# Kernel tuning notes

Hardware: AMD Instinct MI355X
Metric: run time of the kernel (lower is better)

Reference implementation:

```python
import jax, jax.numpy as jnp
import numpy as np

N = 50000      # nodes
E = 800000     # edges per relation
D_IN = 128
D_OUT = 128


def setup_inputs() -> dict:
    key = jax.random.key(0)
    ks = jax.random.split(key, 9)
    feat = jax.random.normal(ks[0], (N, D_IN), dtype=jnp.float32)
    src0 = jax.random.randint(ks[1], (E,), 0, N)
    dst0 = jax.random.randint(ks[2], (E,), 0, N)
    src1 = jax.random.randint(ks[3], (E,), 0, N)
    dst1 = jax.random.randint(ks[4], (E,), 0, N)
    s = 1.0 / np.sqrt(D_IN)
    W0 = jax.random.uniform(ks[5], (D_IN, D_OUT), jnp.float32, -s, s)
    b0 = jax.random.uniform(ks[6], (D_OUT,), jnp.float32, -s, s)
    W1 = jax.random.uniform(ks[7], (D_IN, D_OUT), jnp.float32, -s, s)
    b1 = jax.random.uniform(ks[8], (D_OUT,), jnp.float32, -s, s)
    return {"feat": feat, "W0": W0, "b0": b0, "W1": W1, "b1": b1,
            "src0": src0, "dst0": dst0, "src1": src1, "dst1": dst1}


def _rel_mean(Wh, src, dst):
    # copy_u('Wh','m') + mean('m','h'): gather src features, mean over in-edges per dst
    msg = Wh[src]                                  # [E, D_OUT] irregular gather
    summ = jax.ops.segment_sum(msg, dst, num_segments=N)
    cnt = jax.ops.segment_sum(jnp.ones((msg.shape[0],), Wh.dtype), dst, num_segments=N)
    return summ / jnp.maximum(cnt, 1.0)[:, None]   # isolated dst nodes -> 0


def reference(feat, W0, b0, W1, b1, src0, dst0, src1, dst1):
    Wh0 = feat @ W0 + b0                           # per-etype linear on src features
    Wh1 = feat @ W1 + b1
    h = _rel_mean(Wh0, src0, dst0) + _rel_mean(Wh1, src1, dst1)  # 'sum' cross-reducer
    return h
```

## Files before the change

### kernel.cpp

```cpp
#include <hip/hip_runtime.h>
#include <hip/hip_fp16.h>

#define N_NODES 50000
#define N_EDGES 800000
#define DIM 128
#define NPB 64
#define NB 782
#define BCAP 1344
#define CHUNK 4096
#define GROWS 64

__global__ __launch_bounds__(512) void bin_kernel(
    const int* __restrict__ src0, const int* __restrict__ dst0,
    const int* __restrict__ src1, const int* __restrict__ dst1,
    int* __restrict__ gcur, unsigned* __restrict__ staging) {
    __shared__ int hist[NB], base[NB], curs[NB], gbase[NB];
    __shared__ int wtot[8], wbase[8];
    __shared__ unsigned stageRec[CHUNK];
    __shared__ int tgt[CHUNK];

    int t = threadIdx.x;
    const int nchunks = (N_EDGES + CHUNK - 1) / CHUNK;
    int rel = blockIdx.x >= nchunks;
    int ci  = rel ? blockIdx.x - nchunks : blockIdx.x;
    const int* src = rel ? src1 : src0;
    const int* dst = rel ? dst1 : dst0;
    int e0 = ci * CHUNK;
    int n = N_EDGES - e0; if (n > CHUNK) n = CHUNK;

    for (int i = t; i < NB; i += 512) hist[i] = 0;
    __syncthreads();

    for (int i = t; i < n; i += 512) {
        int d = dst[e0 + i];
        atomicAdd(&hist[d >> 6], 1);
    }
    __syncthreads();

    {
        int i0 = t * 2;
        int s0 = (i0 < NB) ? hist[i0] : 0;
        int s1 = (i0 + 1 < NB) ? hist[i0 + 1] : 0;
        int v = s0 + s1;
        int lane = t & 63, w = t >> 6;
        int x = v;
        #pragma unroll
        for (int dd = 1; dd < 64; dd <<= 1) {
            int u = __shfl_up(x, dd);
            if (lane >= dd) x += u;
        }
        if (lane == 63) wtot[w] = x;
        __syncthreads();
        if (t == 0) {
            int s = 0;
            #pragma unroll
            for (int j = 0; j < 8; ++j) { wbase[j] = s; s += wtot[j]; }
        }
        __syncthreads();
        int excl = wbase[w] + x - v;
        if (i0 < NB)     { base[i0] = excl;          curs[i0] = excl; }
        if (i0 + 1 < NB) { base[i0 + 1] = excl + s0; curs[i0 + 1] = excl + s0; }
    }
    __syncthreads();
    for (int i = t; i < NB; i += 512) {
        int c = hist[i];
        gbase[i] = c ? atomicAdd(&gcur[rel * NB + i], c) : 0;
    }
    __syncthreads();

    for (int i = t; i < n; i += 512) {
        int s = src[e0 + i];
        int d = dst[e0 + i];
        int bkt = d >> 6;
        int pos = atomicAdd(&curs[bkt], 1);
        int j = pos - base[bkt];
        int go = gbase[bkt] + j;
        stageRec[pos] = ((unsigned)s << 6) | (unsigned)(d & 63);
        tgt[pos] = (go < BCAP) ? (rel * NB + bkt) * BCAP + go : -1;
    }
    __syncthreads();

    for (int i = t; i < n; i += 512) {
        int a = tgt[i];
        if (a >= 0) staging[a] = stageRec[i];
    }
}

__global__ __launch_bounds__(256) void gemm_kernel(const float* __restrict__ feat,
                                                   const float* __restrict__ W0,
                                                   const float* __restrict__ b0,
                                                   const float* __restrict__ W1,
                                                   const float* __restrict__ b1,
                                                   __half* __restrict__ Wh0,
                                                   __half* __restrict__ Wh1) {
    __shared__ float fs[GROWS][DIM];
    int tx = threadIdx.x;
    int ty = threadIdx.y;
    int t = ty * 32 + tx;
    int row0 = blockIdx.x * GROWS;
    int nrows = N_NODES - row0; if (nrows > GROWS) nrows = GROWS;

    const float4* fsrc = (const float4*)(feat + (size_t)row0 * DIM);
    float4* fdst = (float4*)(&fs[0][0]);
    int nf4 = nrows * (DIM / 4);
    #pragma unroll
    for (int j = 0; j < 8; ++j) {
        int idx = t + j * 256;
        if (idx < nf4) fdst[idx] = fsrc[idx];
    }
    __syncthreads();

    int c4 = tx * 4;
    float4 acc0[8], acc1[8];
    #pragma unroll
    for (int r = 0; r < 8; ++r) {
        acc0[r] = make_float4(0.f, 0.f, 0.f, 0.f);
        acc1[r] = make_float4(0.f, 0.f, 0.f, 0.f);
    }

    #pragma unroll 2
    for (int k = 0; k < DIM; ++k) {
        float4 w0 = *(const float4*)(W0 + k * DIM + c4);
        float4 w1 = *(const float4*)(W1 + k * DIM + c4);
        #pragma unroll
        for (int r = 0; r < 8; ++r) {
            float f = fs[ty * 8 + r][k];
            acc0[r].x += f * w0.x; acc0[r].y += f * w0.y;
            acc0[r].z += f * w0.z; acc0[r].w += f * w0.w;
            acc1[r].x += f * w1.x; acc1[r].y += f * w1.y;
            acc1[r].z += f * w1.z; acc1[r].w += f * w1.w;
        }
    }

    float4 bb0 = *(const float4*)(b0 + c4);
    float4 bb1 = *(const float4*)(b1 + c4);
    #pragma unroll
    for (int r = 0; r < 8; ++r) {
        int row = row0 + ty * 8 + r;
        if (row < N_NODES) {
            __half2 p0 = __floats2half2_rn(acc0[r].x + bb0.x, acc0[r].y + bb0.y);
            __half2 p1 = __floats2half2_rn(acc0[r].z + bb0.z, acc0[r].w + bb0.w);
            uint2 pk;
            pk.x = *(unsigned*)&p0; pk.y = *(unsigned*)&p1;
            *(uint2*)(Wh0 + (size_t)row * DIM + c4) = pk;
            p0 = __floats2half2_rn(acc1[r].x + bb1.x, acc1[r].y + bb1.y);
            p1 = __floats2half2_rn(acc1[r].z + bb1.z, acc1[r].w + bb1.w);
            pk.x = *(unsigned*)&p0; pk.y = *(unsigned*)&p1;
            *(uint2*)(Wh1 + (size_t)row * DIM + c4) = pk;
        }
    }
}

__device__ inline float4 cvt8(uint2 r) {
    __half2 h0, h1;
    *(unsigned*)&h0 = r.x; *(unsigned*)&h1 = r.y;
    float2 f0 = __half22float2(h0), f1 = __half22float2(h1);
    return make_float4(f0.x, f0.y, f1.x, f1.y);
}

__global__ __launch_bounds__(512) void pull2_kernel(
    const unsigned* __restrict__ staging, const int* __restrict__ gcur,
    const __half* __restrict__ Wh0, const __half* __restrict__ Wh1,
    float* __restrict__ out) {
    __shared__ int srt[2][BCAP];
    __shared__ int hist2[2][NPB], off2[2][NPB], cur2[2][NPB];

    int b = blockIdx.x;
    int t = threadIdx.x;
    int nb0 = b * NPB;
    int n_nodes = N_NODES - nb0; if (n_nodes > NPB) n_nodes = NPB;

    int c0 = gcur[b];       if (c0 > BCAP) c0 = BCAP;
    int c1 = gcur[NB + b];  if (c1 > BCAP) c1 = BCAP;
    const unsigned* st0 = staging + (size_t)b * BCAP;
    const unsigned* st1 = staging + (size_t)(NB + b) * BCAP;

    if (t < 2 * NPB) ((int*)hist2)[t] = 0;
    __syncthreads();

    for (int i = t; i < c0; i += 512) atomicAdd(&hist2[0][st0[i] & 63], 1);
    for (int i = t; i < c1; i += 512) atomicAdd(&hist2[1][st1[i] & 63], 1);
    __syncthreads();

    if (t < 2 * NPB) {
        int r = t >> 6, l = t & 63;
        int v = hist2[r][l];
        int x = v;
        #pragma unroll
        for (int dd = 1; dd < 64; dd <<= 1) {
            int u = __shfl_up(x, dd);
            if (l >= dd) x += u;
        }
        off2[r][l] = x - v;
        cur2[r][l] = x - v;
    }
    __syncthreads();

    for (int i = t; i < c0; i += 512) {
        unsigned rec = st0[i];
        int pos = atomicAdd(&cur2[0][rec & 63], 1);
        srt[0][pos] = (int)(rec >> 6);
    }
    for (int i = t; i < c1; i += 512) {
        unsigned rec = st1[i];
        int pos = atomicAdd(&cur2[1][rec & 63], 1);
        srt[1][pos] = (int)(rec >> 6);
    }
    __syncthreads();

    int wv = t >> 6, lane = t & 63;
    int hf = lane >> 5;
    int col = (lane & 31) * 4;
    for (int l = wv; l < n_nodes; l += 8) {
        float4 o4 = make_float4(0.f, 0.f, 0.f, 0.f);
        #pragma unroll
        for (int r = 0; r < 2; ++r) {
            const __half* Wh = r ? Wh1 : Wh0;
            int c = hist2[r][l], ob = off2[r][l];
            float4 a = make_float4(0.f, 0.f, 0.f, 0.f);
            float4 bb = make_float4(0.f, 0.f, 0.f, 0.f);
            int i = 0;
            for (; i + 8 <= c; i += 8) {
                int s0 = srt[r][ob + i + hf];
                int s1 = srt[r][ob + i + 2 + hf];
                int s2 = srt[r][ob + i + 4 + hf];
                int s3 = srt[r][ob + i + 6 + hf];
                float4 v0 = cvt8(*(const uint2*)(Wh + (size_t)s0 * DIM + col));
                float4 v1 = cvt8(*(const uint2*)(Wh + (size_t)s1 * DIM + col));
                float4 v2 = cvt8(*(const uint2*)(Wh + (size_t)s2 * DIM + col));
                float4 v3 = cvt8(*(const uint2*)(Wh + (size_t)s3 * DIM + col));
                a.x += v0.x; a.y += v0.y; a.z += v0.z; a.w += v0.w;
                bb.x += v1.x; bb.y += v1.y; bb.z += v1.z; bb.w += v1.w;
                a.x += v2.x; a.y += v2.y; a.z += v2.z; a.w += v2.w;
                bb.x += v3.x; bb.y += v3.y; bb.z += v3.z; bb.w += v3.w;
            }
            for (; i < c; i += 2) {
                int e = i + hf;
                if (e < c) {
                    int s = srt[r][ob + e];
                    float4 v = cvt8(*(const uint2*)(Wh + (size_t)s * DIM + col));
                    a.x += v.x; a.y += v.y; a.z += v.z; a.w += v.w;
                }
            }
            a.x += bb.x; a.y += bb.y; a.z += bb.z; a.w += bb.w;
            float f = 1.0f / (float)(c > 0 ? c : 1);
            o4.x += a.x * f; o4.y += a.y * f; o4.z += a.z * f; o4.w += a.w * f;
        }
        o4.x += __shfl_xor(o4.x, 32);
        o4.y += __shfl_xor(o4.y, 32);
        o4.z += __shfl_xor(o4.z, 32);
        o4.w += __shfl_xor(o4.w, 32);
        if (hf == 0) {
            *(float4*)(out + (size_t)(nb0 + l) * DIM + col) = o4;
        }
    }
}

extern "C" void kernel_launch(void* const* d_in, const int* in_sizes, int n_in,
                              void* d_out, int out_size, void* d_ws, size_t ws_size,
                              hipStream_t stream) {
    const float* feat = (const float*)d_in[0];
    const float* W0   = (const float*)d_in[1];
    const float* b0   = (const float*)d_in[2];
    const float* W1   = (const float*)d_in[3];
    const float* b1   = (const float*)d_in[4];
    const int* src0   = (const int*)d_in[5];
    const int* dst0   = (const int*)d_in[6];
    const int* src1   = (const int*)d_in[7];
    const int* dst1   = (const int*)d_in[8];
    float* out = (float*)d_out;

    char* ws = (char*)d_ws;
    size_t o = 0;
    auto carve = [&](size_t bytes) {
        void* p = ws + o;
        o += (bytes + 255) & ~size_t(255);
        return p;
    };
    __half* Wh0      = (__half*)carve(sizeof(__half) * N_NODES * DIM);
    __half* Wh1      = (__half*)carve(sizeof(__half) * N_NODES * DIM);
    unsigned* staging = (unsigned*)carve(sizeof(unsigned) * 2 * NB * BCAP);
    int* gcur        = (int*)carve(sizeof(int) * 2 * NB);

    hipMemsetAsync(gcur, 0, sizeof(int) * 2 * NB, stream);

    const int nchunks = (N_EDGES + CHUNK - 1) / CHUNK;
    bin_kernel<<<2 * nchunks, 512, 0, stream>>>(src0, dst0, src1, dst1,
                                                gcur, staging);
    gemm_kernel<<<(N_NODES + GROWS - 1) / GROWS, dim3(32, 8), 0, stream>>>(
        feat, W0, b0, W1, b1, Wh0, Wh1);
    pull2_kernel<<<NB, 512, 0, stream>>>(staging, gcur, Wh0, Wh1, out);
}
```

Baseline: 241.9 us.

## Use MFMA fp16 for the linear layer and split aggregation blocks in half

The scalar FP32 GEMM becomes an MFMA 16x16x32 f16 kernel. A new pack kernel converts W0/W1 into fragment-ordered half8 tiles, feature rows are converted to fp16 fragments in LDS, and outputs are staged through LDS for coalesced stores. The pull kernel now launches two 256-thread blocks per 64-node bucket, each handling 32 destination nodes and filtering records by half, which raises block count but reads each staging bucket twice. Input features are now rounded to fp16 before the multiply, which costs precision, and the smaller HCAP may drop edges if one half overflows.

Result: faster. 195.6 us (-19.1%).

```diff
diff --git a/kernel.cpp b/kernel.cpp
--- a/kernel.cpp
+++ b/kernel.cpp
@@ -7,8 +7,11 @@
 #define NPB 64
 #define NB 782
 #define BCAP 1344
+#define HCAP 768
 #define CHUNK 4096
-#define GROWS 64
+
+typedef _Float16 half8 __attribute__((ext_vector_type(8)));
+typedef float f32x4 __attribute__((ext_vector_type(4)));
 
 __global__ __launch_bounds__(512) void bin_kernel(
     const int* __restrict__ src0, const int* __restrict__ dst0,
@@ -86,67 +89,118 @@
     }
 }
 
+__global__ __launch_bounds__(256) void wpack_kernel(const float* __restrict__ W0,
+                                                    const float* __restrict__ W1,
+                                                    half8* __restrict__ Bp) {
+    int tid = blockIdx.x * 256 + threadIdx.x;
+    int lane = tid & 63;
+    int nt = (tid >> 6) & 7;
+    int ks = (tid >> 9) & 3;
+    int rel = (tid >> 11) & 1;
+    const float* W = rel ? W1 : W0;
+    int g = lane >> 4, r = lane & 15;
+    int n = nt * 16 + r;
+    half8 h;
+    #pragma unroll
+    for (int j = 0; j < 8; ++j) {
+        int k = ks * 32 + (j >> 2) * 16 + g * 4 + (j & 3);
+        h[j] = (_Float16)W[k * DIM + n];
+    }
+    Bp[tid] = h;
+}
+
 __global__ __launch_bounds__(256) void gemm_kernel(const float* __restrict__ feat,
-                                                   const float* __restrict__ W0,
+                                                   const half8* __restrict__ Bp,
                                                    const float* __restrict__ b0,
-                                                   const float* __restrict__ W1,
                                                    const float* __restrict__ b1,
                                                    __half* __restrict__ Wh0,
                                                    __half* __restrict__ Wh1) {
-    __shared__ float fs[GROWS][DIM];
-    int tx = threadIdx.x;
-    int ty = threadIdx.y;
-    int t = ty * 32 + tx;
-    int row0 = blockIdx.x * GROWS;
-    int nrows = N_NODES - row0; if (nrows > GROWS) nrows = GROWS;
+    __shared__ __align__(16) _Float16 Afrag[4 * 4 * 64 * 8];
+    __shared__ __align__(16) __half Otile[64 * DIM];
+
+    int t = threadIdx.x;
+    int row0 = blockIdx.x * 64;
+    int totalRows = N_NODES - row0; if (totalRows > 64) totalRows = 64;
 
     const float4* fsrc = (const float4*)(feat + (size_t)row0 * DIM);
-    float4* fdst = (float4*)(&fs[0][0]);
-    int nf4 = nrows * (DIM / 4);
-    #pragma unroll
-    for (int j = 0; j < 8; ++j) {
-        int idx = t + j * 256;
-        if (idx < nf4) fdst[idx] = fsrc[idx];
-    }
-    __syncthreads();
-
-    int c4 = tx * 4;
-    float4 acc0[8], acc1[8];
-    #pragma unroll
-    for (int r = 0; r < 8; ++r) {
-        acc0[r] = make_float4(0.f, 0.f, 0.f, 0.f);
-        acc1[r] = make_float4(0.f, 0.f, 0.f, 0.f);
-    }
-
-    #pragma unroll 2
-    for (int k = 0; k < DIM; ++k) {
-        float4 w0 = *(const float4*)(W0 + k * DIM + c4);
-        float4 w1 = *(const float4*)(W1 + k * DIM + c4);
-        #pragma unroll
-        for (int r = 0; r < 8; ++r) {
-            float f = fs[ty * 8 + r][k];
-            acc0[r].x += f * w0.x; acc0[r].y += f * w0.y;
-            acc0[r].z += f * w0.z; acc0[r].w += f * w0.w;
-            acc1[r].x += f * w1.x; acc1[r].y += f * w1.y;
-            acc1[r].z += f * w1.z; acc1[r].w += f * w1.w;
-        }
-    }
-
-    float4 bb0 = *(const float4*)(b0 + c4);
-    float4 bb1 = *(const float4*)(b1 + c4);
-    #pragma unroll
-    for (int r = 0; r < 8; ++r) {
-        int row = row0 + ty * 8 + r;
-        if (row < N_NODES) {
-            __half2 p0 = __floats2half2_rn(acc0[r].x + bb0.x, acc0[r].y + bb0.y);
-            __half2 p1 = __floats2half2_rn(acc0[r].z + bb0.z, acc0[r].w + bb0.w);
-            uint2 pk;
-            pk.x = *(unsigned*)&p0; pk.y = *(unsigned*)&p1;
-            *(uint2*)(Wh0 + (size_t)row * DIM + c4) = pk;
-            p0 = __floats2half2_rn(acc1[r].x + bb1.x, acc1[r].y + bb1.y);
-            p1 = __floats2half2_rn(acc1[r].z + bb1.z, acc1[r].w + bb1.w);
-            pk.x = *(unsigned*)&p0; pk.y = *(unsigned*)&p1;
-            *(uint2*)(Wh1 + (size_t)row * DIM + c4) = pk;
+    #pragma unroll
+    for (int i = 0; i < 8; ++i) {
+        int e = t + i * 256;
+        int row = e >> 5;
+        int kq = e & 31;
+        float4 v = (row < totalRows) ? fsrc[e] : make_float4(0.f, 0.f, 0.f, 0.f);
+        int ks = kq >> 3;
+        int g  = kq & 3;
+        int hi = (kq >> 2) & 1;
+        int wv = row >> 4, r = row & 15;
+        union { _Float16 h[4]; uint2 u; } p;
+        p.h[0] = (_Float16)v.x; p.h[1] = (_Float16)v.y;
+        p.h[2] = (_Float16)v.z; p.h[3] = (_Float16)v.w;
+        *(uint2*)((char*)Afrag + (((wv * 4 + ks) * 64 + g * 16 + r) * 16 + hi * 8)) = p.u;
+    }
+    __syncthreads();
+
+    int wv = t >> 6, l = t & 63;
+    half8 a[4];
+    #pragma unroll
+    for (int ks = 0; ks < 4; ++ks)
+        a[ks] = ((const half8*)Afrag)[(wv * 4 + ks) * 64 + l];
+
+    f32x4 acc0[8], acc1[8];
+    #pragma unroll
+    for (int nt = 0; nt < 8; ++nt) { acc0[nt] = (f32x4)0.f; acc1[nt] = (f32x4)0.f; }
+
+    #pragma unroll
+    for (int nt = 0; nt < 8; ++nt) {
+        #pragma unroll
+        for (int ks = 0; ks < 4; ++ks) {
+            half8 bf0 = Bp[(ks * 8 + nt) * 64 + l];
+            acc0[nt] = __builtin_amdgcn_mfma_f32_16x16x32_f16(a[ks], bf0, acc0[nt], 0, 0, 0);
+            half8 bf1 = Bp[((4 + ks) * 8 + nt) * 64 + l];
+            acc1[nt] = __builtin_amdgcn_mfma_f32_16x16x32_f16(a[ks], bf1, acc1[nt], 0, 0, 0);
+        }
+    }
+
+    int cR = l & 15, rG = l >> 4;
+    #pragma unroll
+    for (int nt = 0; nt < 8; ++nt) {
+        float bias = b0[nt * 16 + cR];
+        #pragma unroll
+        for (int reg = 0; reg < 4; ++reg) {
+            int rowL = rG * 4 + reg;
+            Otile[(wv * 16 + rowL) * DIM + nt * 16 + cR] = __float2half(acc0[nt][reg] + bias);
+        }
+    }
+    __syncthreads();
+    {
+        const uint4* ot = (const uint4*)Otile;
+        uint4* dst = (uint4*)(Wh0 + (size_t)row0 * DIM);
+        #pragma unroll
+        for (int i = 0; i < 4; ++i) {
+            int idx = t + i * 256;
+            int row = idx >> 4;
+            if (row < totalRows) dst[idx] = ot[idx];
+        }
+    }
+    __syncthreads();
+    #pragma unroll
+    for (int nt = 0; nt < 8; ++nt) {
+        float bias = b1[nt * 16 + cR];
+        #pragma unroll
+        for (int reg = 0; reg < 4; ++reg) {
+            int rowL = rG * 4 + reg;
+            Otile[(wv * 16 + rowL) * DIM + nt * 16 + cR] = __float2half(acc1[nt][reg] + bias);
+        }
+    }
+    __syncthreads();
+    {
+        const uint4* ot = (const uint4*)Otile;
+        uint4* dst = (uint4*)(Wh1 + (size_t)row0 * DIM);
+        #pragma unroll
+        for (int i = 0; i < 4; ++i) {
+            int idx = t + i * 256;
+            int row = idx >> 4;
+            if (row < totalRows) dst[idx] = ot[idx];
         }
     }
 }
@@ -158,36 +212,45 @@
     return make_float4(f0.x, f0.y, f1.x, f1.y);
 }
 
-__global__ __launch_bounds__(512) void pull2_kernel(
+__global__ __launch_bounds__(256) void pull2_kernel(
     const unsigned* __restrict__ staging, const int* __restrict__ gcur,
     const __half* __restrict__ Wh0, const __half* __restrict__ Wh1,
     float* __restrict__ out) {
-    __shared__ int srt[2][BCAP];
-    __shared__ int hist2[2][NPB], off2[2][NPB], cur2[2][NPB];
-
-    int b = blockIdx.x;
+    __shared__ int srt[2][HCAP];
+    __shared__ int hist2[2][32], off2[2][32], cur2[2][32];
+
+    int blk = blockIdx.x;
+    int b = blk >> 1, half = blk & 1;
     int t = threadIdx.x;
-    int nb0 = b * NPB;
-    int n_nodes = N_NODES - nb0; if (n_nodes > NPB) n_nodes = NPB;
+    int nb0 = b * NPB + half * 32;
+    int n_nodes = N_NODES - nb0;
+    if (n_nodes > 32) n_nodes = 32;
+    if (n_nodes < 0) n_nodes = 0;
 
     int c0 = gcur[b];       if (c0 > BCAP) c0 = BCAP;
     int c1 = gcur[NB + b];  if (c1 > BCAP) c1 = BCAP;
     const unsigned* st0 = staging + (size_t)b * BCAP;
     const unsigned* st1 = staging + (size_t)(NB + b) * BCAP;
 
-    if (t < 2 * NPB) ((int*)hist2)[t] = 0;
-    __syncthreads();
-
-    for (int i = t; i < c0; i += 512) atomicAdd(&hist2[0][st0[i] & 63], 1);
-    for (int i = t; i < c1; i += 512) atomicAdd(&hist2[1][st1[i] & 63], 1);
-    __syncthreads();
-
-    if (t < 2 * NPB) {
-        int r = t >> 6, l = t & 63;
+    if (t < 64) ((int*)hist2)[t] = 0;
+    __syncthreads();
+
+    for (int i = t; i < c0; i += 256) {
+        unsigned rec = st0[i]; int d = rec & 63;
+        if ((d >> 5) == half) atomicAdd(&hist2[0][d & 31], 1);
+    }
+    for (int i = t; i < c1; i += 256) {
+        unsigned rec = st1[i]; int d = rec & 63;
+        if ((d >> 5) == half) atomicAdd(&hist2[1][d & 31], 1);
+    }
+    __syncthreads();
+
+    if (t < 64) {
+        int r = t >> 5, l = t & 31;
         int v = hist2[r][l];
         int x = v;
         #pragma unroll
-        for (int dd = 1; dd < 64; dd <<= 1) {
+        for (int dd = 1; dd < 32; dd <<= 1) {
             int u = __shfl_up(x, dd);
             if (l >= dd) x += u;
         }
@@ -196,22 +259,26 @@
     }
     __syncthreads();
 
-    for (int i = t; i < c0; i += 512) {
-        unsigned rec = st0[i];
-        int pos = atomicAdd(&cur2[0][rec & 63], 1);
-        srt[0][pos] = (int)(rec >> 6);
-    }
-    for (int i = t; i < c1; i += 512) {
-        unsigned rec = st1[i];
-        int pos = atomicAdd(&cur2[1][rec & 63], 1);
-        srt[1][pos] = (int)(rec >> 6);
+    for (int i = t; i < c0; i += 256) {
+        unsigned rec = st0[i]; int d = rec & 63;
+        if ((d >> 5) == half) {
+            int pos = atomicAdd(&cur2[0][d & 31], 1);
+            if (pos < HCAP) srt[0][pos] = (int)(rec >> 6);
+        }
+    }
+    for (int i = t; i < c1; i += 256) {
+        unsigned rec = st1[i]; int d = rec & 63;
+        if ((d >> 5) == half) {
+            int pos = atomicAdd(&cur2[1][d & 31], 1);
+            if (pos < HCAP) srt[1][pos] = (int)(rec >> 6);
+        }
     }
     __syncthreads();
 
     int wv = t >> 6, lane = t & 63;
     int hf = lane >> 5;
     int col = (lane & 31) * 4;
-    for (int l = wv; l < n_nodes; l += 8) {
+    for (int l = wv; l < n_nodes; l += 4) {
         float4 o4 = make_float4(0.f, 0.f, 0.f, 0.f);
         #pragma unroll
         for (int r = 0; r < 2; ++r) {
@@ -277,17 +344,19 @@
         o += (bytes + 255) & ~size_t(255);
         return p;
     };
-    __half* Wh0      = (__half*)carve(sizeof(__half) * N_NODES * DIM);
-    __half* Wh1      = (__half*)carve(sizeof(__half) * N_NODES * DIM);
+    __half* Wh0       = (__half*)carve(sizeof(__half) * N_NODES * DIM);
+    __half* Wh1       = (__half*)carve(sizeof(__half) * N_NODES * DIM);
     unsigned* staging = (unsigned*)carve(sizeof(unsigned) * 2 * NB * BCAP);
-    int* gcur        = (int*)carve(sizeof(int) * 2 * NB);
+    half8* Bp         = (half8*)carve(sizeof(half8) * 4096);
+    int* gcur         = (int*)carve(sizeof(int) * 2 * NB);
 
     hipMemsetAsync(gcur, 0, sizeof(int) * 2 * NB, stream);
 
     const int nchunks = (N_EDGES + CHUNK - 1) / CHUNK;
+    wpack_kernel<<<16, 256, 0, stream>>>(W0, W1, Bp);
     bin_kernel<<<2 * nchunks, 512, 0, stream>>>(src0, dst0, src1, dst1,
                                                 gcur, staging);
-    gemm_kernel<<<(N_NODES + GROWS - 1) / GROWS, dim3(32, 8), 0, stream>>>(
-        feat, W0, b0, W1, b1, Wh0, Wh1);
-    pull2_kernel<<<NB, 512, 0, stream>>>(staging, gcur, Wh0, Wh1, out);
-}
+    gemm_kernel<<<(N_NODES + 63) / 64, 256, 0, stream>>>(feat, Bp, b0, b1,
+                                                         Wh0, Wh1);
+    pull2_kernel<<<2 * NB, 256, 0, stream>>>(staging, gcur, Wh0, Wh1, out);
+}
```
